# Kernel tuning notes

Hardware: AMD Instinct MI355X
Metric: run time of the kernel (lower is better)

## Reference

```python
import jax, jax.numpy as jnp
import numpy as np

N_PATCHES = 32
N_POINTS = 2048
N_SIGMA = 1


def setup_inputs() -> dict:
    key = jax.random.key(0)
    pcs = jax.random.normal(key, (8192, N_POINTS, 3), dtype=jnp.float32)
    return {"pcs": pcs}


def reference(pcs):
    B = pcs.shape[0]
    P = N_PATCHES
    n = N_POINTS // P  # points per patch
    x = pcs.reshape(B, P, n, 3)
    means = x.mean(axis=2)                 # [B, P, 3]
    stds = x.std(axis=2, ddof=1)           # [B, P, 3] (torch std is unbiased)
    # all-pairs |mean_i - mean_j| and std_i + std_j, [B, P, P, 3]
    delta = jnp.abs(means[:, :, None, :] - means[:, None, :, :])
    ssum = stds[:, :, None, :] + stds[:, None, :, :]
    rep = jax.nn.relu(ssum * N_SIGMA - delta)
    norms = jnp.sqrt(jnp.sum(rep * rep, axis=-1))  # [B, P, P]
    # original loops over i <= j (diagonal included): upper triangle incl. diag
    mask = jnp.triu(jnp.ones((P, P), dtype=norms.dtype))
    n_pairs = P * (P + 1) // 2
    return jnp.sum(norms * mask) / (n_pairs * B)
```

## Files before the change

kernel.cpp:

```cpp
#include <hip/hip_runtime.h>

#define NPTS 2048
#define NPATCH 32
#define PTS_PER_PATCH 64
#define FLOATS_PER_BATCH (NPTS*3)
#define N_PAIRS 528.0f
#define BATCHES_PER_BLOCK 4

__global__ __launch_bounds__(256) void patch_stage1(
    const float* __restrict__ pcs, float* __restrict__ ws) {
  const int tid = threadIdx.x;
  const int p   = tid >> 3;
  const int s   = tid & 7;

  __shared__ float smean[NPATCH][4];
  __shared__ float sstd[NPATCH][4];

  float acc = 0.f;

#pragma unroll
  for (int m = 0; m < BATCHES_PER_BLOCK; ++m) {
    const int b = blockIdx.x + gridDim.x * m;
    const float4* p4 =
        (const float4*)(pcs + (size_t)b * FLOATS_PER_BATCH) + 48 * p + s;

    float4 v[6];
#pragma unroll
    for (int k = 0; k < 6; ++k) v[k] = p4[8 * k];

    float L0 = 0.f, L1 = 0.f, L2 = 0.f;
    float Q0 = 0.f, Q1 = 0.f, Q2 = 0.f;

#define ACC(k, a, bb, c)                                          \
    { float x = v[k].x, y = v[k].y, z = v[k].z, w = v[k].w;       \
      L##a += x + w; Q##a += x * x + w * w;                       \
      L##bb += y;    Q##bb += y * y;                              \
      L##c += z;     Q##c += z * z; }
    ACC(0, 0, 1, 2)
    ACC(1, 2, 0, 1)
    ACC(2, 1, 2, 0)
    ACC(3, 0, 1, 2)
    ACC(4, 2, 0, 1)
    ACC(5, 1, 2, 0)
#undef ACC

    float sx, sy, sz, sxx, syy, szz;
    const int s3 = s % 3;
    if (s3 == 0)      { sx = L0; sy = L1; sz = L2; sxx = Q0; syy = Q1; szz = Q2; }
    else if (s3 == 1) { sx = L2; sy = L0; sz = L1; sxx = Q2; syy = Q0; szz = Q1; }
    else              { sx = L1; sy = L2; sz = L0; sxx = Q1; syy = Q2; szz = Q0; }

#pragma unroll
    for (int off = 4; off >= 1; off >>= 1) {
      sx  += __shfl_down(sx,  off, 8);
      sy  += __shfl_down(sy,  off, 8);
      sz  += __shfl_down(sz,  off, 8);
      sxx += __shfl_down(sxx, off, 8);
      syy += __shfl_down(syy, off, 8);
      szz += __shfl_down(szz, off, 8);
    }

    if (m > 0) __syncthreads();

    if (s == 0) {
      const float inv_n = 1.0f / PTS_PER_PATCH;
      const float inv_nm1 = 1.0f / (PTS_PER_PATCH - 1);
      smean[p][0] = sx * inv_n; smean[p][1] = sy * inv_n; smean[p][2] = sz * inv_n;
      sstd[p][0] = sqrtf(fmaxf((sxx - sx * sx * inv_n) * inv_nm1, 0.f));
      sstd[p][1] = sqrtf(fmaxf((syy - sy * sy * inv_n) * inv_nm1, 0.f));
      sstd[p][2] = sqrtf(fmaxf((szz - sz * sz * inv_n) * inv_nm1, 0.f));
    }
    __syncthreads();

#pragma unroll
    for (int r = 0; r < 4; ++r) {
      const int q = tid + 256 * r;
      const int i = q >> 5;
      const int j = q & 31;
      if (i <= j) {
        float rx = fmaxf((sstd[i][0] + sstd[j][0]) - fabsf(smean[i][0] - smean[j][0]), 0.f);
        float ry = fmaxf((sstd[i][1] + sstd[j][1]) - fabsf(smean[i][1] - smean[j][1]), 0.f);
        float rz = fmaxf((sstd[i][2] + sstd[j][2]) - fabsf(smean[i][2] - smean[j][2]), 0.f);
        acc += sqrtf(rx * rx + ry * ry + rz * rz);
      }
    }
  }

#pragma unroll
  for (int off = 32; off >= 1; off >>= 1) acc += __shfl_down(acc, off);
  __shared__ float wpart[4];
  if ((tid & 63) == 0) wpart[tid >> 6] = acc;
  __syncthreads();
  if (tid == 0) ws[blockIdx.x] = wpart[0] + wpart[1] + wpart[2] + wpart[3];
}

__global__ __launch_bounds__(256) void patch_stage2(
    const float* __restrict__ ws, float* __restrict__ out, int n, float scale) {
  float acc = 0.f;
  for (int i = threadIdx.x; i < n; i += 256) acc += ws[i];
#pragma unroll
  for (int off = 32; off >= 1; off >>= 1) acc += __shfl_down(acc, off);
  __shared__ float wpart[4];
  if ((threadIdx.x & 63) == 0) wpart[threadIdx.x >> 6] = acc;
  __syncthreads();
  if (threadIdx.x == 0) out[0] = (wpart[0] + wpart[1] + wpart[2] + wpart[3]) * scale;
}

extern "C" void kernel_launch(void* const* d_in, const int* in_sizes, int n_in,
                              void* d_out, int out_size, void* d_ws, size_t ws_size,
                              hipStream_t stream) {
  const float* pcs = (const float*)d_in[0];
  float* out = (float*)d_out;
  float* ws  = (float*)d_ws;

  const int B = in_sizes[0] / FLOATS_PER_BATCH;
  const int nblocks = B / BATCHES_PER_BLOCK;
  const float scale = 1.0f / (N_PAIRS * (float)B);

  patch_stage1<<<nblocks, 256, 0, stream>>>(pcs, ws);
  patch_stage2<<<1, 256, 0, stream>>>(ws, out, nblocks, scale);
}
```

Measured before the change: 273.8 us.

## Fuse reduction stages with atomics, prefetch next batch, use double-buffered LDS

Merges the two-kernel reduction into one kernel that adds its block partial sums to the output with atomicAdd, after a memset of the output. It also prefetches the next batch's float4 loads into registers while the current batch is processed, and double-buffers the per-patch stats in LDS so only one barrier is needed per batch. Pairwise work is redistributed: each thread uses its own patch stats plus 4 rows of j, and weights off-diagonal pairs by 0.5 to exploit symmetry. Risks include higher register pressure, nondeterministic atomic summation order, and an extra memset launch.

```diff
diff --git a/kernel.cpp b/kernel.cpp
--- a/kernel.cpp
+++ b/kernel.cpp
@@ -4,38 +4,55 @@
 #define NPATCH 32
 #define PTS_PER_PATCH 64
 #define FLOATS_PER_BATCH (NPTS*3)
+#define F4_PER_BATCH (FLOATS_PER_BATCH/4)
 #define N_PAIRS 528.0f
-#define BATCHES_PER_BLOCK 4
+#define BPB 4
 
-__global__ __launch_bounds__(256) void patch_stage1(
-    const float* __restrict__ pcs, float* __restrict__ ws) {
+__device__ __forceinline__ void lds_barrier() {
+  __builtin_amdgcn_sched_barrier(0);
+  asm volatile("s_waitcnt lgkmcnt(0)" ::: "memory");
+  __builtin_amdgcn_s_barrier();
+  __builtin_amdgcn_sched_barrier(0);
+}
+
+__global__ __launch_bounds__(256) void patch_fused(
+    const float* __restrict__ pcs, float* __restrict__ out, float scale) {
   const int tid = threadIdx.x;
   const int p   = tid >> 3;
   const int s   = tid & 7;
 
-  __shared__ float smean[NPATCH][4];
-  __shared__ float sstd[NPATCH][4];
+  __shared__ float sms[2][NPATCH][6];
+  __shared__ float wpart[4];
 
+  const size_t bstride = (size_t)gridDim.x * F4_PER_BATCH;
+  const float4* pb = (const float4*)pcs + (size_t)blockIdx.x * F4_PER_BATCH
+                     + 48 * p + s;
+
+  float4 vb[2][6];
   float acc = 0.f;
 
 #pragma unroll
-  for (int m = 0; m < BATCHES_PER_BLOCK; ++m) {
-    const int b = blockIdx.x + gridDim.x * m;
-    const float4* p4 =
-        (const float4*)(pcs + (size_t)b * FLOATS_PER_BATCH) + 48 * p + s;
+  for (int k = 0; k < 6; ++k) vb[0][k] = pb[8 * k];
 
-    float4 v[6];
 #pragma unroll
-    for (int k = 0; k < 6; ++k) v[k] = p4[8 * k];
+  for (int m = 0; m < BPB; ++m) {
+    const int cur = m & 1;
+
+    if (m + 1 < BPB) {
+      const float4* pn = pb + (size_t)(m + 1) * bstride;
+#pragma unroll
+      for (int k = 0; k < 6; ++k) vb[cur ^ 1][k] = pn[8 * k];
+    }
 
     float L0 = 0.f, L1 = 0.f, L2 = 0.f;
     float Q0 = 0.f, Q1 = 0.f, Q2 = 0.f;
 
-#define ACC(k, a, bb, c)                                          \
-    { float x = v[k].x, y = v[k].y, z = v[k].z, w = v[k].w;       \
-      L##a += x + w; Q##a += x * x + w * w;                       \
-      L##bb += y;    Q##bb += y * y;                              \
-      L##c += z;     Q##c += z * z; }
+#define ACC(k, a, bb, c)                                                 \
+    { float x = vb[cur][k].x, y = vb[cur][k].y,                          \
+            z = vb[cur][k].z, w = vb[cur][k].w;                          \
+      L##a += x + w; Q##a = fmaf(x, x, Q##a); Q##a = fmaf(w, w, Q##a);   \
+      L##bb += y;    Q##bb = fmaf(y, y, Q##bb);                          \
+      L##c += z;     Q##c = fmaf(z, z, Q##c); }
     ACC(0, 0, 1, 2)
     ACC(1, 2, 0, 1)
     ACC(2, 1, 2, 0)
@@ -51,59 +68,50 @@
     else              { sx = L1; sy = L2; sz = L0; sxx = Q1; syy = Q2; szz = Q0; }
 
 #pragma unroll
-    for (int off = 4; off >= 1; off >>= 1) {
-      sx  += __shfl_down(sx,  off, 8);
-      sy  += __shfl_down(sy,  off, 8);
-      sz  += __shfl_down(sz,  off, 8);
-      sxx += __shfl_down(sxx, off, 8);
-      syy += __shfl_down(syy, off, 8);
-      szz += __shfl_down(szz, off, 8);
+    for (int off = 1; off <= 4; off <<= 1) {
+      sx  += __shfl_xor(sx,  off, 8);
+      sy  += __shfl_xor(sy,  off, 8);
+      sz  += __shfl_xor(sz,  off, 8);
+      sxx += __shfl_xor(sxx, off, 8);
+      syy += __shfl_xor(syy, off, 8);
+      szz += __shfl_xor(szz, off, 8);
     }
 
-    if (m > 0) __syncthreads();
+    const float inv_n   = 1.0f / PTS_PER_PATCH;
+    const float inv_nm1 = 1.0f / (PTS_PER_PATCH - 1);
+    const float mx = sx * inv_n, my = sy * inv_n, mz = sz * inv_n;
+    const float tx = sqrtf(fmaxf((sxx - sx * sx * inv_n) * inv_nm1, 0.f));
+    const float ty = sqrtf(fmaxf((syy - sy * sy * inv_n) * inv_nm1, 0.f));
+    const float tz = sqrtf(fmaxf((szz - sz * sz * inv_n) * inv_nm1, 0.f));
 
     if (s == 0) {
-      const float inv_n = 1.0f / PTS_PER_PATCH;
-      const float inv_nm1 = 1.0f / (PTS_PER_PATCH - 1);
-      smean[p][0] = sx * inv_n; smean[p][1] = sy * inv_n; smean[p][2] = sz * inv_n;
-      sstd[p][0] = sqrtf(fmaxf((sxx - sx * sx * inv_n) * inv_nm1, 0.f));
-      sstd[p][1] = sqrtf(fmaxf((syy - sy * sy * inv_n) * inv_nm1, 0.f));
-      sstd[p][2] = sqrtf(fmaxf((szz - sz * sz * inv_n) * inv_nm1, 0.f));
+      float* row = &sms[cur][p][0];
+      row[0] = mx; row[1] = my; row[2] = mz;
+      row[3] = tx; row[4] = ty; row[5] = tz;
     }
-    __syncthreads();
+    lds_barrier();
 
 #pragma unroll
     for (int r = 0; r < 4; ++r) {
-      const int q = tid + 256 * r;
-      const int i = q >> 5;
-      const int j = q & 31;
-      if (i <= j) {
-        float rx = fmaxf((sstd[i][0] + sstd[j][0]) - fabsf(smean[i][0] - smean[j][0]), 0.f);
-        float ry = fmaxf((sstd[i][1] + sstd[j][1]) - fabsf(smean[i][1] - smean[j][1]), 0.f);
-        float rz = fmaxf((sstd[i][2] + sstd[j][2]) - fabsf(smean[i][2] - smean[j][2]), 0.f);
-        acc += sqrtf(rx * rx + ry * ry + rz * rz);
-      }
+      const int j = s + 8 * r;
+      const float* row = &sms[cur][j][0];
+      const float dx = fabsf(mx - row[0]);
+      const float dy = fabsf(my - row[1]);
+      const float dz = fabsf(mz - row[2]);
+      const float rx = fmaxf((tx + row[3]) - dx, 0.f);
+      const float ry = fmaxf((ty + row[4]) - dy, 0.f);
+      const float rz = fmaxf((tz + row[5]) - dz, 0.f);
+      const float nrm = sqrtf(fmaf(rx, rx, fmaf(ry, ry, rz * rz)));
+      acc += (p == j ? 1.0f : 0.5f) * nrm;
     }
   }
 
 #pragma unroll
   for (int off = 32; off >= 1; off >>= 1) acc += __shfl_down(acc, off);
-  __shared__ float wpart[4];
   if ((tid & 63) == 0) wpart[tid >> 6] = acc;
   __syncthreads();
-  if (tid == 0) ws[blockIdx.x] = wpart[0] + wpart[1] + wpart[2] + wpart[3];
-}
-
-__global__ __launch_bounds__(256) void patch_stage2(
-    const float* __restrict__ ws, float* __restrict__ out, int n, float scale) {
-  float acc = 0.f;
-  for (int i = threadIdx.x; i < n; i += 256) acc += ws[i];
-#pragma unroll
-  for (int off = 32; off >= 1; off >>= 1) acc += __shfl_down(acc, off);
-  __shared__ float wpart[4];
-  if ((threadIdx.x & 63) == 0) wpart[threadIdx.x >> 6] = acc;
-  __syncthreads();
-  if (threadIdx.x == 0) out[0] = (wpart[0] + wpart[1] + wpart[2] + wpart[3]) * scale;
+  if (tid == 0)
+    atomicAdd(out, (wpart[0] + wpart[1] + wpart[2] + wpart[3]) * scale);
 }
 
 extern "C" void kernel_launch(void* const* d_in, const int* in_sizes, int n_in,
@@ -111,12 +119,11 @@
                               hipStream_t stream) {
   const float* pcs = (const float*)d_in[0];
   float* out = (float*)d_out;
-  float* ws  = (float*)d_ws;
 
   const int B = in_sizes[0] / FLOATS_PER_BATCH;
-  const int nblocks = B / BATCHES_PER_BLOCK;
+  const int nblocks = B / BPB;
   const float scale = 1.0f / (N_PAIRS * (float)B);
 
-  patch_stage1<<<nblocks, 256, 0, stream>>>(pcs, ws);
-  patch_stage2<<<1, 256, 0, stream>>>(ws, out, nblocks, scale);
+  hipMemsetAsync(out, 0, sizeof(float), stream);
+  patch_fused<<<nblocks, 256, 0, stream>>>(pcs, out, scale);
 }
```

After: 272.5 us. About the same (-0.5%).
